# Performance work log

Measured on AMD Instinct MI355X. Metric: run time of the kernel, lower is better.

The kernel has to match this reference:

```python
import jax, jax.numpy as jnp
import numpy as np

N_HEAD, D_K, D_V, D_MODEL = 16, 64, 64, 1024
B, S = 2, 2048


def setup_inputs() -> dict:
    key = jax.random.key(0)
    ks = jax.random.split(key, 9)
    Q = jax.random.normal(ks[0], (B, S, D_MODEL), jnp.float32)
    K = jax.random.normal(ks[1], (B, S, D_MODEL), jnp.float32)
    V = jax.random.normal(ks[2], (B, S, D_MODEL), jnp.float32)
    mask = jax.random.randint(ks[3], (B, 1, S), 0, 2) > 0  # bool, ~half valid
    # xavier-normal-ish std for (d_model, d_k) fan
    std_qk = (2.0 / (D_MODEL + D_K)) ** 0.5
    std_v = (2.0 / (D_MODEL + D_V)) ** 0.5
    Wq = std_qk * jax.random.normal(ks[4], (N_HEAD, D_MODEL, D_K), jnp.float32)
    Wk = std_qk * jax.random.normal(ks[5], (N_HEAD, D_MODEL, D_K), jnp.float32)
    Wv = std_v * jax.random.normal(ks[6], (N_HEAD, D_MODEL, D_V), jnp.float32)
    bound = (6.0 / (N_HEAD * D_V)) ** 0.5  # kaiming_uniform-ish
    Wo = jax.random.uniform(ks[7], (N_HEAD * D_V, D_MODEL), jnp.float32, -bound, bound)
    return {"Q": Q, "K": K, "V": V, "Wq": Wq, "Wk": Wk, "Wv": Wv, "Wo": Wo, "mask": mask}


def reference(Q, K, V, Wq, Wk, Wv, Wo, mask):
    n_head, d_model, d_k = Wq.shape
    d_v = Wv.shape[-1]
    b, sq, _ = Q.shape
    sk = K.shape[1]
    # Per-head projections; torch cat over heads == leading head axis here.
    q = jnp.einsum('bsd,hdk->hbsk', Q, Wq)  # (H,B,Sq,dk)
    k = jnp.einsum('bsd,hdk->hbsk', K, Wk)  # (H,B,Sk,dk)
    v = jnp.einsum('bsd,hdv->hbsv', V, Wv)  # (H,B,Sk,dv)
    scores = jnp.einsum('hbqk,hbsk->hbqs', q, k) / (d_k ** 0.5)
    m = mask[None]  # (1,B,1,Sk), broadcasts over heads and queries
    scores = jnp.where(m, scores, -1e9)
    attn = jax.nn.softmax(scores, axis=-1)
    attn = jnp.where(m, attn, 0.0)
    out = jnp.einsum('hbqs,hbsv->hbqv', attn, v)  # (H,B,Sq,dv)
    # torch: split along batch*head dim then cat on feature dim -> head-major feature concat
    out = jnp.transpose(out, (1, 2, 0, 3)).reshape(b, sq, n_head * d_v)
    out = out @ Wo  # (B,Sq,d_model); dropout is identity in eval
    attns = attn.reshape(n_head * b, sq, sk)
    return out, attns
```

## Files before the change

kernel.cpp:

```cpp
#include <hip/hip_runtime.h>
#include <hip/hip_bf16.h>

typedef __attribute__((ext_vector_type(8))) short short8;
typedef __attribute__((ext_vector_type(4))) float floatx4;

#define H 16
#define BB 2
#define SS 2048
#define DM 1024
#define DK 64

__device__ __forceinline__ unsigned short f2bf(float f) {
  union { float f; unsigned int u; } x; x.f = f;
  unsigned int r = (x.u + 0x7fffu + ((x.u >> 16) & 1u)) >> 16;
  return (unsigned short)r;
}
__device__ __forceinline__ float bf2f(unsigned short h) {
  union { unsigned int u; float f; } x; x.u = (unsigned int)h << 16;
  return x.f;
}

__global__ __launch_bounds__(256) void convert_qkv(
    const float* __restrict__ Q, const float* __restrict__ K, const float* __restrict__ V,
    unsigned short* __restrict__ Qb, unsigned short* __restrict__ Kb,
    unsigned short* __restrict__ Vb) {
  const float* in; unsigned short* out;
  int z = blockIdx.y;
  if (z == 0)      { in = Q; out = Qb; }
  else if (z == 1) { in = K; out = Kb; }
  else             { in = V; out = Vb; }
  size_t i = ((size_t)blockIdx.x * 256 + threadIdx.x) * 4;
  float4 v = *(const float4*)&in[i];
  ushort4 o;
  o.x = f2bf(v.x); o.y = f2bf(v.y); o.z = f2bf(v.z); o.w = f2bf(v.w);
  *(ushort4*)&out[i] = o;
}

__global__ __launch_bounds__(256) void repack_w(
    const float* __restrict__ Wq, const float* __restrict__ Wk,
    const float* __restrict__ Wv, const float* __restrict__ Wo,
    unsigned short* __restrict__ Wq_t, unsigned short* __restrict__ Wk_t,
    unsigned short* __restrict__ Wv_t, unsigned short* __restrict__ Wo_t) {
  int z = blockIdx.z;
  int bx = blockIdx.x, by = blockIdx.y;
  int t = threadIdx.x;
  const float* in;
  unsigned short* out;
  if (z == 0)      { in = Wq; out = Wq_t; }
  else if (z == 1) { in = Wk; out = Wk_t; }
  else if (z == 2) { in = Wv; out = Wv_t; }
  else             { in = Wo; out = Wo_t; }
  #pragma unroll
  for (int i = 0; i < 16; i++) {
    int o = t + i * 256;
    int r = o >> 6, cloc = o & 63;
    if (z < 3) {
      out[(bx * 64 + r) * 1024 + by * 64 + cloc] =
          f2bf(in[bx * 65536 + (by * 64 + cloc) * 64 + r]);
    } else {
      out[(bx * 64 + r) * 1024 + by * 64 + cloc] =
          f2bf(in[(by * 64 + cloc) * 1024 + bx * 64 + r]);
    }
  }
}

__global__ __launch_bounds__(256) void gemm_bt(
    const unsigned short* __restrict__ A, const unsigned short* __restrict__ Bt,
    unsigned short* __restrict__ C, float* __restrict__ Cf, int M, int N, int K) {
  __shared__ __align__(16) unsigned short a_lds[128 * 32];
  __shared__ __align__(16) unsigned short b_lds[128 * 32];
  const int bn = blockIdx.x * 128, bm = blockIdx.y * 128;
  const int t = threadIdx.x;
  const int wave = t >> 6, lane = t & 63;
  const int quad = lane >> 4, l15 = lane & 15;
  const int wm = (wave & 1) * 64, wn = (wave >> 1) * 64;
  floatx4 acc[4][4] = {};
  for (int kt = 0; kt < K; kt += 32) {
    __syncthreads();
    {
      int c = t;
      #pragma unroll
      for (int it = 0; it < 2; it++, c += 256) {
        int row = c >> 2, col = (c & 3) * 8;
        *(uint4*)&a_lds[row * 32 + col] =
            *(const uint4*)&A[(size_t)(bm + row) * K + kt + col];
      }
      c = t;
      #pragma unroll
      for (int it = 0; it < 2; it++, c += 256) {
        int row = c >> 2, col = (c & 3) * 8;
        *(uint4*)&b_lds[row * 32 + col] =
            *(const uint4*)&Bt[(size_t)(bn + row) * K + kt + col];
      }
    }
    __syncthreads();
    short8 af[4], bfr[4];
    #pragma unroll
    for (int mt = 0; mt < 4; mt++)
      af[mt] = *(const short8*)&a_lds[(wm + mt * 16 + l15) * 32 + quad * 8];
    #pragma unroll
    for (int nt = 0; nt < 4; nt++)
      bfr[nt] = *(const short8*)&b_lds[(wn + nt * 16 + l15) * 32 + quad * 8];
    #pragma unroll
    for (int mt = 0; mt < 4; mt++)
      #pragma unroll
      for (int nt = 0; nt < 4; nt++)
        acc[mt][nt] = __builtin_amdgcn_mfma_f32_16x16x32_bf16(af[mt], bfr[nt], acc[mt][nt], 0, 0, 0);
  }
  if (Cf) {
    #pragma unroll
    for (int mt = 0; mt < 4; mt++)
      #pragma unroll
      for (int nt = 0; nt < 4; nt++)
        #pragma unroll
        for (int r = 0; r < 4; r++) {
          int row = bm + wm + mt * 16 + quad * 4 + r;
          int col = bn + wn + nt * 16 + l15;
          Cf[(size_t)row * N + col] = acc[mt][nt][r];
        }
  } else {
    #pragma unroll
    for (int mt = 0; mt < 4; mt++)
      #pragma unroll
      for (int nt = 0; nt < 4; nt++)
        #pragma unroll
        for (int r = 0; r < 4; r++) {
          int row = bm + wm + mt * 16 + quad * 4 + r;
          int col = bn + wn + nt * 16 + l15;
          C[(size_t)row * N + col] = f2bf(acc[mt][nt][r]);
        }
  }
}

__global__ __launch_bounds__(256) void attn_kernel(
    const unsigned short* __restrict__ q2, const unsigned short* __restrict__ k2,
    const unsigned short* __restrict__ vt, const void* __restrict__ mask,
    float* __restrict__ attns, unsigned short* __restrict__ ctx) {
  __shared__ __align__(16) unsigned short k_lds[128 * 64];
  __shared__ __align__(16) unsigned short vt_lds[64 * 128];
  __shared__ __align__(16) unsigned short pq_lds[64 * 128];
  __shared__ float maskmul[SS];
  __shared__ float rowsum_inv[64];
  __shared__ int s_fp32, s_byte2, s_gt1;
  const int qt = blockIdx.x, b = blockIdx.y, h = blockIdx.z;
  const int t = threadIdx.x;
  const int wave = t >> 6, lane = t & 63;
  const int quad = lane >> 4, l15 = lane & 15;

  if (t == 0) { s_fp32 = 1; s_byte2 = 0; s_gt1 = 0; }
  __syncthreads();
  {
    const unsigned int* mw = (const unsigned int*)mask;
    int f_fp32 = 1, f_byte2 = 0, f_gt1 = 0;
    for (int i = t; i < 1024; i += 256) {
      unsigned int w = mw[i];
      if (!(w == 0u || w == 0x3F800000u)) f_fp32 = 0;
      if (((w & 0xFFu) > 1u) || (((w >> 8) & 0xFFu) > 1u) ||
          (((w >> 16) & 0xFFu) > 1u) || ((w >> 24) > 1u)) f_byte2 = 1;
      if (w > 1u) f_gt1 = 1;
    }
    if (!f_fp32) atomicAnd(&s_fp32, 0);
    if (f_byte2) atomicOr(&s_byte2, 1);
    if (f_gt1)  atomicOr(&s_gt1, 1);
  }
  __syncthreads();
  {
    const unsigned int*   mw = (const unsigned int*)mask;
    const unsigned short* mh = (const unsigned short*)mask;
    const unsigned char*  mb = (const unsigned char*)mask;
    int mode = s_fp32 ? 0 : (s_byte2 ? 1 : (s_gt1 ? 2 : 3));
    for (int i = t; i < SS; i += 256) {
      int idx = b * SS + i;
      bool mv;
      if (mode == 0)      mv = mw[idx] != 0u;
      else if (mode == 1) mv = mh[idx] != 0u;
      else if (mode == 2) mv = mb[idx] != 0u;
      else                mv = mw[idx] != 0u;
      maskmul[i] = mv ? 1.0f : 0.0f;
    }
  }

  {
    int c = t;
    #pragma unroll
    for (int it = 0; it < 2; it++, c += 256) {
      int r = c >> 3, cc = (c & 7) * 8;
      *(uint4*)&pq_lds[r * 64 + cc] =
          *(const uint4*)&q2[(size_t)(b * SS + qt * 64 + r) * DM + h * DK + cc];
    }
  }
  __syncthreads();
  short8 aq0 = *(const short8*)&pq_lds[(wave * 16 + l15) * 64 + quad * 8];
  short8 aq1 = *(const short8*)&pq_lds[(wave * 16 + l15) * 64 + 32 + quad * 8];

  const float cexp = 0.18033688011112042f;
  float rs[4] = {0.f, 0.f, 0.f, 0.f};

  for (int kt = 0; kt < 16; kt++) {
    __syncthreads();
    int c = t;
    #pragma unroll
    for (int it = 0; it < 4; it++, c += 256) {
      int r = c >> 3, cc = (c & 7) * 8;
      *(uint4*)&k_lds[r * 64 + cc] =
          *(const uint4*)&k2[(size_t)(b * SS + kt * 128 + r) * DM + h * DK + cc];
    }
    __syncthreads();
    #pragma unroll
    for (int ct = 0; ct < 8; ct++) {
      floatx4 s = {};
      short8 bk0 = *(const short8*)&k_lds[(ct * 16 + l15) * 64 + quad * 8];
      short8 bk1 = *(const short8*)&k_lds[(ct * 16 + l15) * 64 + 32 + quad * 8];
      s = __builtin_amdgcn_mfma_f32_16x16x32_bf16(aq0, bk0, s, 0, 0, 0);
      s = __builtin_amdgcn_mfma_f32_16x16x32_bf16(aq1, bk1, s, 0, 0, 0);
      float m = maskmul[kt * 128 + ct * 16 + l15];
      #pragma unroll
      for (int r = 0; r < 4; r++) rs[r] += m * exp2f(s[r] * cexp);
    }
  }
  #pragma unroll
  for (int r = 0; r < 4; r++) {
    rs[r] += __shfl_xor(rs[r], 1);
    rs[r] += __shfl_xor(rs[r], 2);
    rs[r] += __shfl_xor(rs[r], 4);
    rs[r] += __shfl_xor(rs[r], 8);
  }
  if (l15 == 0) {
    #pragma unroll
    for (int r = 0; r < 4; r++)
      rowsum_inv[wave * 16 + quad * 4 + r] = rs[r] > 0.f ? 1.0f / rs[r] : 0.f;
  }

  floatx4 cacc[4] = {};
  for (int kt = 0; kt < 16; kt++) {
    __syncthreads();
    {
      int c = t;
      #pragma unroll
      for (int it = 0; it < 4; it++, c += 256) {
        int r = c >> 3, cc = (c & 7) * 8;
        *(uint4*)&k_lds[r * 64 + cc] =
            *(const uint4*)&k2[(size_t)(b * SS + kt * 128 + r) * DM + h * DK + cc];
      }
      c = t;
      #pragma unroll
      for (int it = 0; it < 4; it++, c += 256) {
        int n = c >> 4, cc = (c & 15) * 8;
        *(uint4*)&vt_lds[n * 128 + cc] =
            *(const uint4*)&vt[(size_t)(h * DK + n) * (BB * SS) + b * SS + kt * 128 + cc];
      }
    }
    __syncthreads();
    float rinv[4];
    #pragma unroll
    for (int r = 0; r < 4; r++) rinv[r] = rowsum_inv[wave * 16 + quad * 4 + r];
    #pragma unroll
    for (int ct = 0; ct < 8; ct++) {
      floatx4 s = {};
      short8 bk0 = *(const short8*)&k_lds[(ct * 16 + l15) * 64 + quad * 8];
      short8 bk1 = *(const short8*)&k_lds[(ct * 16 + l15) * 64 + 32 + quad * 8];
      s = __builtin_amdgcn_mfma_f32_16x16x32_bf16(aq0, bk0, s, 0, 0, 0);
      s = __builtin_amdgcn_mfma_f32_16x16x32_bf16(aq1, bk1, s, 0, 0, 0);
      float m = maskmul[kt * 128 + ct * 16 + l15];
      #pragma unroll
      for (int r = 0; r < 4; r++) {
        float p = m * exp2f(s[r] * cexp) * rinv[r];
        pq_lds[(wave * 16 + quad * 4 + r) * 128 + ct * 16 + l15] = f2bf(p);
      }
    }
    __syncthreads();
    {
      int c = t;
      #pragma unroll
      for (int it = 0; it < 8; it++, c += 256) {
        int r = c >> 5, fc = (c & 31) * 4;
        const unsigned short* src = &pq_lds[r * 128 + fc];
        float4 f;
        f.x = bf2f(src[0]); f.y = bf2f(src[1]);
        f.z = bf2f(src[2]); f.w = bf2f(src[3]);
        *(float4*)&attns[((size_t)(h * BB + b) * SS + qt * 64 + r) * SS + kt * 128 + fc] = f;
      }
    }
    #pragma unroll
    for (int ks = 0; ks < 4; ks++) {
      short8 ap = *(const short8*)&pq_lds[(wave * 16 + l15) * 128 + ks * 32 + quad * 8];
      #pragma unroll
      for (int ct = 0; ct < 4; ct++) {
        short8 bv = *(const short8*)&vt_lds[(ct * 16 + l15) * 128 + ks * 32 + quad * 8];
        cacc[ct] = __builtin_amdgcn_mfma_f32_16x16x32_bf16(ap, bv, cacc[ct], 0, 0, 0);
      }
    }
  }
  #pragma unroll
  for (int ct = 0; ct < 4; ct++)
    #pragma unroll
    for (int r = 0; r < 4; r++) {
      int row = b * SS + qt * 64 + wave * 16 + quad * 4 + r;
      int col = h * DK + ct * 16 + l15;
      ctx[(size_t)row * DM + col] = f2bf(cacc[ct][r]);
    }
}

extern "C" void kernel_launch(void* const* d_in, const int* in_sizes, int n_in,
                              void* d_out, int out_size, void* d_ws, size_t ws_size,
                              hipStream_t stream) {
  (void)in_sizes; (void)n_in; (void)out_size; (void)ws_size;
  const float* Q  = (const float*)d_in[0];
  const float* K  = (const float*)d_in[1];
  const float* V  = (const float*)d_in[2];
  const float* Wq = (const float*)d_in[3];
  const float* Wk = (const float*)d_in[4];
  const float* Wv = (const float*)d_in[5];
  const float* Wo = (const float*)d_in[6];
  const void* mask = d_in[7];

  float* out   = (float*)d_out;
  float* attns = out + (size_t)BB * SS * DM;

  char* ws = (char*)d_ws;
  unsigned short* Qb   = (unsigned short*)(ws);
  unsigned short* Kb   = (unsigned short*)(ws + (size_t)(8u  << 20));
  unsigned short* Vb   = (unsigned short*)(ws + (size_t)(16u << 20));
  unsigned short* q2   = (unsigned short*)(ws + (size_t)(24u << 20));
  unsigned short* k2   = (unsigned short*)(ws + (size_t)(32u << 20));
  unsigned short* vt   = (unsigned short*)(ws + (size_t)(40u << 20));
  unsigned short* ctx  = (unsigned short*)(ws + (size_t)(48u << 20));
  unsigned short* Wq_t = (unsigned short*)(ws + (size_t)(56u << 20));
  unsigned short* Wk_t = (unsigned short*)(ws + (size_t)(58u << 20));
  unsigned short* Wv_t = (unsigned short*)(ws + (size_t)(60u << 20));
  unsigned short* Wo_t = (unsigned short*)(ws + (size_t)(62u << 20));

  convert_qkv<<<dim3(4096, 3), 256, 0, stream>>>(Q, K, V, Qb, Kb, Vb);
  repack_w<<<dim3(16, 16, 4), 256, 0, stream>>>(Wq, Wk, Wv, Wo, Wq_t, Wk_t, Wv_t, Wo_t);
  gemm_bt<<<dim3(8, 32), 256, 0, stream>>>(Qb, Wq_t, q2, nullptr, 4096, 1024, 1024);
  gemm_bt<<<dim3(8, 32), 256, 0, stream>>>(Kb, Wk_t, k2, nullptr, 4096, 1024, 1024);
  gemm_bt<<<dim3(32, 8), 256, 0, stream>>>(Wv_t, Vb, vt, nullptr, 1024, 4096, 1024);
  attn_kernel<<<dim3(32, 2, 16), 256, 0, stream>>>(q2, k2, vt, mask, attns, ctx);
  gemm_bt<<<dim3(8, 32), 256, 0, stream>>>(ctx, Wo_t, nullptr, out, 4096, 1024, 1024);
}
```

Baseline: 880.4 us.

## Fuse attention passes into one, rescale attns afterward, retile GEMM with padded LDS

Result: slower. 1.068 ms (+21.3%).

```diff
diff --git a/kernel.cpp b/kernel.cpp
--- a/kernel.cpp
+++ b/kernel.cpp
@@ -67,51 +67,57 @@
 __global__ __launch_bounds__(256) void gemm_bt(
     const unsigned short* __restrict__ A, const unsigned short* __restrict__ Bt,
     unsigned short* __restrict__ C, float* __restrict__ Cf, int M, int N, int K) {
-  __shared__ __align__(16) unsigned short a_lds[128 * 32];
-  __shared__ __align__(16) unsigned short b_lds[128 * 32];
-  const int bn = blockIdx.x * 128, bm = blockIdx.y * 128;
+  __shared__ __align__(16) unsigned short a_lds[128 * 72];
+  __shared__ __align__(16) unsigned short b_lds[64 * 72];
+  const int bn = blockIdx.x * 64, bm = blockIdx.y * 128;
   const int t = threadIdx.x;
   const int wave = t >> 6, lane = t & 63;
   const int quad = lane >> 4, l15 = lane & 15;
-  const int wm = (wave & 1) * 64, wn = (wave >> 1) * 64;
-  floatx4 acc[4][4] = {};
-  for (int kt = 0; kt < K; kt += 32) {
+  const int wm = (wave & 1) * 64, wn = (wave >> 1) * 32;
+  floatx4 acc[4][2] = {};
+  for (int kt = 0; kt < K; kt += 64) {
     __syncthreads();
     {
       int c = t;
       #pragma unroll
+      for (int it = 0; it < 4; it++, c += 256) {
+        int row = c >> 3, col = (c & 7) * 8;
+        *(uint4*)&a_lds[row * 72 + col] =
+            *(const uint4*)&A[(size_t)(bm + row) * K + kt + col];
+      }
+      c = t;
+      #pragma unroll
       for (int it = 0; it < 2; it++, c += 256) {
-        int row = c >> 2, col = (c & 3) * 8;
-        *(uint4*)&a_lds[row * 32 + col] =
-            *(const uint4*)&A[(size_t)(bm + row) * K + kt + col];
-      }
-      c = t;
-      #pragma unroll
-      for (int it = 0; it < 2; it++, c += 256) {
-        int row = c >> 2, col = (c & 3) * 8;
-        *(uint4*)&b_lds[row * 32 + col] =
+        int row = c >> 3, col = (c & 7) * 8;
+        *(uint4*)&b_lds[row * 72 + col] =
             *(const uint4*)&Bt[(size_t)(bn + row) * K + kt + col];
       }
     }
     __syncthreads();
-    short8 af[4], bfr[4];
+    short8 af0[4], af1[4], bf0[2], bf1[2];
+    #pragma unroll
+    for (int mt = 0; mt < 4; mt++) {
+      af0[mt] = *(const short8*)&a_lds[(wm + mt * 16 + l15) * 72 + quad * 8];
+      af1[mt] = *(const short8*)&a_lds[(wm + mt * 16 + l15) * 72 + 32 + quad * 8];
+    }
+    #pragma unroll
+    for (int nt = 0; nt < 2; nt++) {
+      bf0[nt] = *(const short8*)&b_lds[(wn + nt * 16 + l15) * 72 + quad * 8];
+      bf1[nt] = *(const short8*)&b_lds[(wn + nt * 16 + l15) * 72 + 32 + quad * 8];
+    }
     #pragma unroll
     for (int mt = 0; mt < 4; mt++)
-      af[mt] = *(const short8*)&a_lds[(wm + mt * 16 + l15) * 32 + quad * 8];
-    #pragma unroll
-    for (int nt = 0; nt < 4; nt++)
-      bfr[nt] = *(const short8*)&b_lds[(wn + nt * 16 + l15) * 32 + quad * 8];
+      #pragma unroll
+      for (int nt = 0; nt < 2; nt++) {
+        acc[mt][nt] = __builtin_amdgcn_mfma_f32_16x16x32_bf16(af0[mt], bf0[nt], acc[mt][nt], 0, 0, 0);
+        acc[mt][nt] = __builtin_amdgcn_mfma_f32_16x16x32_bf16(af1[mt], bf1[nt], acc[mt][nt], 0, 0, 0);
+      }
+  }
+  if (Cf) {
     #pragma unroll
     for (int mt = 0; mt < 4; mt++)
       #pragma unroll
-      for (int nt = 0; nt < 4; nt++)
-        acc[mt][nt] = __builtin_amdgcn_mfma_f32_16x16x32_bf16(af[mt], bfr[nt], acc[mt][nt], 0, 0, 0);
-  }
-  if (Cf) {
-    #pragma unroll
-    for (int mt = 0; mt < 4; mt++)
-      #pragma unroll
-      for (int nt = 0; nt < 4; nt++)
+      for (int nt = 0; nt < 2; nt++)
         #pragma unroll
         for (int r = 0; r < 4; r++) {
           int row = bm + wm + mt * 16 + quad * 4 + r;
@@ -122,7 +128,7 @@
     #pragma unroll
     for (int mt = 0; mt < 4; mt++)
       #pragma unroll
-      for (int nt = 0; nt < 4; nt++)
+      for (int nt = 0; nt < 2; nt++)
         #pragma unroll
         for (int r = 0; r < 4; r++) {
           int row = bm + wm + mt * 16 + quad * 4 + r;
@@ -136,9 +142,9 @@
     const unsigned short* __restrict__ q2, const unsigned short* __restrict__ k2,
     const unsigned short* __restrict__ vt, const void* __restrict__ mask,
     float* __restrict__ attns, unsigned short* __restrict__ ctx) {
-  __shared__ __align__(16) unsigned short k_lds[128 * 64];
-  __shared__ __align__(16) unsigned short vt_lds[64 * 128];
-  __shared__ __align__(16) unsigned short pq_lds[64 * 128];
+  __shared__ __align__(16) unsigned short k_lds[128 * 72];
+  __shared__ __align__(16) unsigned short vt_lds[64 * 136];
+  __shared__ __align__(16) unsigned short pq_lds[64 * 136];
   __shared__ float maskmul[SS];
   __shared__ float rowsum_inv[64];
   __shared__ int s_fp32, s_byte2, s_gt1;
@@ -185,39 +191,77 @@
     #pragma unroll
     for (int it = 0; it < 2; it++, c += 256) {
       int r = c >> 3, cc = (c & 7) * 8;
-      *(uint4*)&pq_lds[r * 64 + cc] =
+      *(uint4*)&k_lds[r * 72 + cc] =
           *(const uint4*)&q2[(size_t)(b * SS + qt * 64 + r) * DM + h * DK + cc];
     }
   }
   __syncthreads();
-  short8 aq0 = *(const short8*)&pq_lds[(wave * 16 + l15) * 64 + quad * 8];
-  short8 aq1 = *(const short8*)&pq_lds[(wave * 16 + l15) * 64 + 32 + quad * 8];
+  short8 aq0 = *(const short8*)&k_lds[(wave * 16 + l15) * 72 + quad * 8];
+  short8 aq1 = *(const short8*)&k_lds[(wave * 16 + l15) * 72 + 32 + quad * 8];
 
   const float cexp = 0.18033688011112042f;
   float rs[4] = {0.f, 0.f, 0.f, 0.f};
+  floatx4 cacc[4] = {};
+  const size_t attn_base = ((size_t)(h * BB + b) * SS + qt * 64) * SS;
 
   for (int kt = 0; kt < 16; kt++) {
     __syncthreads();
-    int c = t;
-    #pragma unroll
-    for (int it = 0; it < 4; it++, c += 256) {
-      int r = c >> 3, cc = (c & 7) * 8;
-      *(uint4*)&k_lds[r * 64 + cc] =
-          *(const uint4*)&k2[(size_t)(b * SS + kt * 128 + r) * DM + h * DK + cc];
+    {
+      int c = t;
+      #pragma unroll
+      for (int it = 0; it < 4; it++, c += 256) {
+        int r = c >> 3, cc = (c & 7) * 8;
+        *(uint4*)&k_lds[r * 72 + cc] =
+            *(const uint4*)&k2[(size_t)(b * SS + kt * 128 + r) * DM + h * DK + cc];
+      }
+      c = t;
+      #pragma unroll
+      for (int it = 0; it < 4; it++, c += 256) {
+        int n = c >> 4, cc = (c & 15) * 8;
+        *(uint4*)&vt_lds[n * 136 + cc] =
+            *(const uint4*)&vt[(size_t)(h * DK + n) * (BB * SS) + b * SS + kt * 128 + cc];
+      }
     }
     __syncthreads();
     #pragma unroll
     for (int ct = 0; ct < 8; ct++) {
       floatx4 s = {};
-      short8 bk0 = *(const short8*)&k_lds[(ct * 16 + l15) * 64 + quad * 8];
-      short8 bk1 = *(const short8*)&k_lds[(ct * 16 + l15) * 64 + 32 + quad * 8];
+      short8 bk0 = *(const short8*)&k_lds[(ct * 16 + l15) * 72 + quad * 8];
+      short8 bk1 = *(const short8*)&k_lds[(ct * 16 + l15) * 72 + 32 + quad * 8];
       s = __builtin_amdgcn_mfma_f32_16x16x32_bf16(aq0, bk0, s, 0, 0, 0);
       s = __builtin_amdgcn_mfma_f32_16x16x32_bf16(aq1, bk1, s, 0, 0, 0);
       float m = maskmul[kt * 128 + ct * 16 + l15];
       #pragma unroll
-      for (int r = 0; r < 4; r++) rs[r] += m * exp2f(s[r] * cexp);
-    }
-  }
+      for (int r = 0; r < 4; r++) {
+        float p = m * exp2f(s[r] * cexp);
+        rs[r] += p;
+        pq_lds[(wave * 16 + quad * 4 + r) * 136 + ct * 16 + l15] = f2bf(p);
+      }
+    }
+    __syncthreads();
+    {
+      int c = t;
+      #pragma unroll
+      for (int it = 0; it < 8; it++, c += 256) {
+        int r = c >> 5, fc = (c & 31) * 4;
+        ushort4 u = *(const ushort4*)&pq_lds[r * 136 + fc];
+        float4 f;
+        f.x = bf2f(u.x); f.y = bf2f(u.y);
+        f.z = bf2f(u.z); f.w = bf2f(u.w);
+        *(float4*)&attns[attn_base + (size_t)r * SS + kt * 128 + fc] = f;
+      }
+    }
+    #pragma unroll
+    for (int ks = 0; ks < 4; ks++) {
+      short8 ap = *(const short8*)&pq_lds[(wave * 16 + l15) * 136 + ks * 32 + quad * 8];
+      #pragma unroll
+      for (int ct = 0; ct < 4; ct++) {
+        short8 bv = *(const short8*)&vt_lds[(ct * 16 + l15) * 136 + ks * 32 + quad * 8];
+        cacc[ct] = __builtin_amdgcn_mfma_f32_16x16x32_bf16(ap, bv, cacc[ct], 0, 0, 0);
+      }
+    }
+  }
+
   #pragma unroll
   for (int r = 0; r < 4; r++) {
     rs[r] += __shfl_xor(rs[r], 1);
@@ -230,74 +274,30 @@
     for (int r = 0; r < 4; r++)
       rowsum_inv[wave * 16 + quad * 4 + r] = rs[r] > 0.f ? 1.0f / rs[r] : 0.f;
   }
-
-  floatx4 cacc[4] = {};
-  for (int kt = 0; kt < 16; kt++) {
-    __syncthreads();
-    {
-      int c = t;
-      #pragma unroll
-      for (int it = 0; it < 4; it++, c += 256) {
-        int r = c >> 3, cc = (c & 7) * 8;
-        *(uint4*)&k_lds[r * 64 + cc] =
-            *(const uint4*)&k2[(size_t)(b * SS + kt * 128 + r) * DM + h * DK + cc];
-      }
-      c = t;
-      #pragma unroll
-      for (int it = 0; it < 4; it++, c += 256) {
-        int n = c >> 4, cc = (c & 15) * 8;
-        *(uint4*)&vt_lds[n * 128 + cc] =
-            *(const uint4*)&vt[(size_t)(h * DK + n) * (BB * SS) + b * SS + kt * 128 + cc];
-      }
-    }
-    __syncthreads();
-    float rinv[4];
-    #pragma unroll
-    for (int r = 0; r < 4; r++) rinv[r] = rowsum_inv[wave * 16 + quad * 4 + r];
-    #pragma unroll
-    for (int ct = 0; ct < 8; ct++) {
-      floatx4 s = {};
-      short8 bk0 = *(const short8*)&k_lds[(ct * 16 + l15) * 64 + quad * 8];
-      short8 bk1 = *(const short8*)&k_lds[(ct * 16 + l15) * 64 + 32 + quad * 8];
-      s = __builtin_amdgcn_mfma_f32_16x16x32_bf16(aq0, bk0, s, 0, 0, 0);
-      s = __builtin_amdgcn_mfma_f32_16x16x32_bf16(aq1, bk1, s, 0, 0, 0);
-      float m = maskmul[kt * 128 + ct * 16 + l15];
-      #pragma unroll
-      for (int r = 0; r < 4; r++) {
-        float p = m * exp2f(s[r] * cexp) * rinv[r];
-        pq_lds[(wave * 16 + quad * 4 + r) * 128 + ct * 16 + l15] = f2bf(p);
-      }
-    }
-    __syncthreads();
-    {
-      int c = t;
-      #pragma unroll
-      for (int it = 0; it < 8; it++, c += 256) {
-        int r = c >> 5, fc = (c & 31) * 4;
-        const unsigned short* src = &pq_lds[r * 128 + fc];
-        float4 f;
-        f.x = bf2f(src[0]); f.y = bf2f(src[1]);
-        f.z = bf2f(src[2]); f.w = bf2f(src[3]);
-        *(float4*)&attns[((size_t)(h * BB + b) * SS + qt * 64 + r) * SS + kt * 128 + fc] = f;
-      }
-    }
-    #pragma unroll
-    for (int ks = 0; ks < 4; ks++) {
-      short8 ap = *(const short8*)&pq_lds[(wave * 16 + l15) * 128 + ks * 32 + quad * 8];
-      #pragma unroll
-      for (int ct = 0; ct < 4; ct++) {
-        short8 bv = *(const short8*)&vt_lds[(ct * 16 + l15) * 128 + ks * 32 + quad * 8];
-        cacc[ct] = __builtin_amdgcn_mfma_f32_16x16x32_bf16(ap, bv, cacc[ct], 0, 0, 0);
-      }
-    }
-  }
+  __threadfence_block();
+  __syncthreads();
+
+  {
+    #pragma unroll 4
+    for (int c = t; c < 64 * (SS / 4); c += 256) {
+      int r = c >> 9;
+      int c4 = c & 511;
+      float rv = rowsum_inv[r];
+      float4* p = (float4*)&attns[attn_base + (size_t)r * SS + c4 * 4];
+      float4 f = *p;
+      f.x *= rv; f.y *= rv; f.z *= rv; f.w *= rv;
+      *p = f;
+    }
+  }
+
   #pragma unroll
   for (int ct = 0; ct < 4; ct++)
     #pragma unroll
     for (int r = 0; r < 4; r++) {
+      float rv = rowsum_inv[wave * 16 + quad * 4 + r];
       int row = b * SS + qt * 64 + wave * 16 + quad * 4 + r;
       int col = h * DK + ct * 16 + l15;
-      ctx[(size_t)row * DM + col] = f2bf(cacc[ct][r]);
+      ctx[(size_t)row * DM + col] = f2bf(cacc[ct][r] * rv);
     }
 }
 
@@ -332,9 +332,9 @@
 
   convert_qkv<<<dim3(4096, 3), 256, 0, stream>>>(Q, K, V, Qb, Kb, Vb);
   repack_w<<<dim3(16, 16, 4), 256, 0, stream>>>(Wq, Wk, Wv, Wo, Wq_t, Wk_t, Wv_t, Wo_t);
-  gemm_bt<<<dim3(8, 32), 256, 0, stream>>>(Qb, Wq_t, q2, nullptr, 4096, 1024, 1024);
-  gemm_bt<<<dim3(8, 32), 256, 0, stream>>>(Kb, Wk_t, k2, nullptr, 4096, 1024, 1024);
-  gemm_bt<<<dim3(32, 8), 256, 0, stream>>>(Wv_t, Vb, vt, nullptr, 1024, 4096, 1024);
+  gemm_bt<<<dim3(16, 32), 256, 0, stream>>>(Qb, Wq_t, q2, nullptr, 4096, 1024, 1024);
+  gemm_bt<<<dim3(16, 32), 256, 0, stream>>>(Kb, Wk_t, k2, nullptr, 4096, 1024, 1024);
+  gemm_bt<<<dim3(64, 8), 256, 0, stream>>>(Wv_t, Vb, vt, nullptr, 1024, 4096, 1024);
   attn_kernel<<<dim3(32, 2, 16), 256, 0, stream>>>(q2, k2, vt, mask, attns, ctx);
-  gemm_bt<<<dim3(8, 32), 256, 0, stream>>>(ctx, Wo_t, nullptr, out, 4096, 1024, 1024);
-}
+  gemm_bt<<<dim3(16, 32), 256, 0, stream>>>(ctx, Wo_t, nullptr, out, 4096, 1024, 1024);
+}
```
